# Kernel optimization log

Hardware: AMD Instinct MI355X
Metric: run time of the kernel (lower is better)

Reference implementation:

```python
import jax, jax.numpy as jnp
import numpy as np

NF = 64   # num_feat
DG = 8    # deformable_groups (also conv groups)
B, H, W = 4, 96, 96
K = 9     # 3x3 kernel positions


def _conv(x, w, b, padding=1, dilation=1, groups=1):
    out = jax.lax.conv_general_dilated(
        x, w, (1, 1), [(padding, padding), (padding, padding)],
        rhs_dilation=(dilation, dilation),
        dimension_numbers=('NCHW', 'OIHW', 'NCHW'),
        feature_group_count=groups)
    return out + b[None, :, None, None]


def _lrelu(t):
    return jnp.where(t >= 0, t, 0.1 * t)


def _cat_align(a, b):
    # channel-interleaved concat: [a0,b0,a1,b1,...]
    Bn, k, h, w = a.shape
    return jnp.stack([a, b], axis=2).reshape(Bn, 2 * k, h, w)


def _deform_conv(x, offset, mask, weight, bias, dilation, padding):
    # DCNv2 modulated deformable conv, stride 1.
    Bn, C, h, w = x.shape
    Cpg = C // DG
    off = offset.reshape(Bn, DG, K, 2, h, w)          # (dy, dx) per group/kernel pos
    m = mask.reshape(Bn, DG, K, h, w)
    ky = (jnp.repeat(jnp.arange(3), 3) * dilation - padding).astype(x.dtype)  # (K,)
    kx = (jnp.tile(jnp.arange(3), 3) * dilation - padding).astype(x.dtype)
    hs = jnp.arange(h, dtype=x.dtype)
    ws = jnp.arange(w, dtype=x.dtype)
    py = off[:, :, :, 0] + ky[None, None, :, None, None] + hs[None, None, None, :, None]
    px = off[:, :, :, 1] + kx[None, None, :, None, None] + ws[None, None, None, None, :]
    y0f = jnp.floor(py); x0f = jnp.floor(px)
    ly = (py - y0f)[:, :, None]  # broadcast over Cpg
    lx = (px - x0f)[:, :, None]
    y0 = y0f.astype(jnp.int32); x0 = x0f.astype(jnp.int32)
    xg = x.reshape(Bn, DG, Cpg, h * w)

    def gather(yi, xi):
        inb = ((yi >= 0) & (yi < h) & (xi >= 0) & (xi < w))
        idx = (jnp.clip(yi, 0, h - 1) * w + jnp.clip(xi, 0, w - 1)).reshape(Bn, DG, 1, K * h * w)
        v = jnp.take_along_axis(xg, jnp.broadcast_to(idx, (Bn, DG, Cpg, K * h * w)), axis=3)
        return v.reshape(Bn, DG, Cpg, K, h, w) * inb[:, :, None].astype(x.dtype)

    v00 = gather(y0, x0); v01 = gather(y0, x0 + 1)
    v10 = gather(y0 + 1, x0); v11 = gather(y0 + 1, x0 + 1)
    val = (v00 * (1 - ly) * (1 - lx) + v01 * (1 - ly) * lx
           + v10 * ly * (1 - lx) + v11 * ly * lx) * m[:, :, None]
    sampled = val.reshape(Bn, C, K, h, w)
    out = jnp.einsum('bckhw,ock->bohw', sampled, weight.reshape(weight.shape[0], C, K))
    return out + bias[None, :, None, None]


def _dcn(x, off_feat, om_w, om_b, w, b, dilation):
    pad = dilation  # int(3/2)*dilation
    out = _conv(off_feat, om_w, om_b, padding=pad, dilation=dilation)
    o1, o2, msk = jnp.split(out, 3, axis=1)
    offset = jnp.concatenate([o1, o2], axis=1)
    mask = jax.nn.sigmoid(msk)
    return _deform_conv(x, offset, mask, w, b, dilation, pad)


def setup_inputs() -> dict:
    key = jax.random.key(0)
    ks = iter(jax.random.split(key, 64))
    def rn(shape, s=0.05):
        return jax.random.normal(next(ks), shape, jnp.float32) * s
    d = {}
    d['nbr_feat'] = jax.random.normal(next(ks), (B, NF, H, W), jnp.float32)
    d['ref_feat'] = jax.random.normal(next(ks), (B, NF, H, W), jnp.float32)
    for lv, has3 in [('l3', False), ('l2', True), ('l1', True)]:
        d[f'oc1_w_{lv}'] = rn((NF, 2 * NF // DG, 3, 3)); d[f'oc1_b_{lv}'] = rn((NF,))
        oc2_in = 2 * NF if has3 else NF
        d[f'oc2_w_{lv}'] = rn((NF, oc2_in // DG, 3, 3)); d[f'oc2_b_{lv}'] = rn((NF,))
        if has3:
            d[f'oc3_w_{lv}'] = rn((NF, NF // DG, 3, 3)); d[f'oc3_b_{lv}'] = rn((NF,))
            d[f'fc_w_{lv}'] = rn((NF, 2 * NF // DG, 3, 3)); d[f'fc_b_{lv}'] = rn((NF,))
        d[f'om_w_{lv}'] = rn((DG * 3 * K, NF, 3, 3), 0.01); d[f'om_b_{lv}'] = rn((DG * 3 * K,), 0.01)
        d[f'dcn_w_{lv}'] = rn((NF, NF, 3, 3)); d[f'dcn_b_{lv}'] = rn((NF,))
    d['cas_oc1_w'] = rn((NF, 2 * NF // DG, 3, 3)); d['cas_oc1_b'] = rn((NF,))
    d['cas_oc2_w'] = rn((NF, NF // DG, 3, 3)); d['cas_oc2_b'] = rn((NF,))
    d['cas_om_w'] = rn((DG * 3 * K, NF, 3, 3), 0.01); d['cas_om_b'] = rn((DG * 3 * K,), 0.01)
    d['cas_w'] = rn((NF, NF, 3, 3)); d['cas_b'] = rn((NF,))
    return d


def reference(nbr_feat, ref_feat,
              oc1_w_l3, oc1_b_l3, oc2_w_l3, oc2_b_l3, om_w_l3, om_b_l3, dcn_w_l3, dcn_b_l3,
              oc1_w_l2, oc1_b_l2, oc2_w_l2, oc2_b_l2, oc3_w_l2, oc3_b_l2, fc_w_l2, fc_b_l2,
              om_w_l2, om_b_l2, dcn_w_l2, dcn_b_l2,
              oc1_w_l1, oc1_b_l1, oc2_w_l1, oc2_b_l1, oc3_w_l1, oc3_b_l1, fc_w_l1, fc_b_l1,
              om_w_l1, om_b_l1, dcn_w_l1, dcn_b_l1,
              cas_oc1_w, cas_oc1_b, cas_oc2_w, cas_oc2_b, cas_om_w, cas_om_b, cas_w, cas_b):
    # level 3 (dilation 5)
    off = _lrelu(_conv(_cat_align(nbr_feat, ref_feat), oc1_w_l3, oc1_b_l3, groups=DG))
    off = _lrelu(_conv(off, oc2_w_l3, oc2_b_l3, groups=DG))
    feat = _lrelu(_dcn(nbr_feat, off, om_w_l3, om_b_l3, dcn_w_l3, dcn_b_l3, 5))
    to, tf = off, feat
    # level 2 (dilation 3)
    off = _lrelu(_conv(_cat_align(nbr_feat, ref_feat), oc1_w_l2, oc1_b_l2, groups=DG))
    off = _lrelu(_conv(_cat_align(off, to), oc2_w_l2, oc2_b_l2, groups=DG))
    off = _lrelu(_conv(off, oc3_w_l2, oc3_b_l2, groups=DG))
    feat = _dcn(nbr_feat, off, om_w_l2, om_b_l2, dcn_w_l2, dcn_b_l2, 3)
    feat = _lrelu(_conv(_cat_align(feat, tf), fc_w_l2, fc_b_l2, groups=DG))
    to, tf = off, feat
    # level 1 (dilation 1), no lrelu on feat
    off = _lrelu(_conv(_cat_align(nbr_feat, ref_feat), oc1_w_l1, oc1_b_l1, groups=DG))
    off = _lrelu(_conv(_cat_align(off, to), oc2_w_l1, oc2_b_l1, groups=DG))
    off = _lrelu(_conv(off, oc3_w_l1, oc3_b_l1, groups=DG))
    feat = _dcn(nbr_feat, off, om_w_l1, om_b_l1, dcn_w_l1, dcn_b_l1, 1)
    feat = _conv(_cat_align(feat, tf), fc_w_l1, fc_b_l1, groups=DG)
    # cascade
    off = _cat_align(feat, ref_feat)
    off = _lrelu(_conv(_lrelu(_conv(off, cas_oc1_w, cas_oc1_b, groups=DG)), cas_oc2_w, cas_oc2_b, groups=DG))
    feat = _lrelu(_dcn(feat, off, cas_om_w, cas_om_b, cas_w, cas_b, 1))
    return feat
```

## Files before the change

kernel.cpp:

```cpp
#include <hip/hip_runtime.h>

#define BATCH 4
#define NFEAT 64
#define DGRP 8
#define HH 96
#define WW 96
#define HWP (HH*WW)

typedef short short4a __attribute__((ext_vector_type(4)));
typedef short short8 __attribute__((ext_vector_type(8)));
typedef float f32x4 __attribute__((ext_vector_type(4)));
typedef float f32x16 __attribute__((ext_vector_type(16)));

__device__ inline short f2bf(float f) {
  union { float f; unsigned u; } v; v.f = f;
  unsigned r = v.u + 0x7fff + ((v.u >> 16) & 1);
  return (short)(r >> 16);
}
__device__ inline float bf2f(short s) {
  return __uint_as_float(((unsigned)(unsigned short)s) << 16);
}

__global__ __launch_bounds__(256) void prep_om(
    const float* __restrict__ s0, const float* __restrict__ s1,
    const float* __restrict__ s2, const float* __restrict__ s3,
    short* __restrict__ dst) {
  int gid = blockIdx.x * 256 + threadIdx.x;
  if (gid >= 4 * 147456) return;
  int t = gid / 147456, r = gid % 147456;
  int tile = r / 18432, r2 = r % 18432;
  int kk = r2 / 512, r3 = r2 % 512;
  int lane = r3 / 8, j = r3 % 8;
  int col = lane & 31, half = lane >> 5;
  int oc = tile * 32 + col;
  int k = kk * 16 + half * 8 + j;
  int p = k >> 6, c = k & 63;
  const float* s = (t == 0) ? s0 : (t == 1) ? s1 : (t == 2) ? s2 : s3;
  float v = (oc < 216) ? s[(size_t)oc * 576 + c * 9 + p] : 0.f;
  dst[gid] = f2bf(v);
}

__global__ __launch_bounds__(256) void prep_dcnw(
    const float* __restrict__ s0, const float* __restrict__ s1,
    const float* __restrict__ s2, const float* __restrict__ s3,
    short* __restrict__ dst) {
  int gid = blockIdx.x * 256 + threadIdx.x;
  if (gid >= 4 * 36864) return;
  int t = gid / 36864, r = gid % 36864;
  int tile = r / 18432, r2 = r % 18432;
  int kk = r2 / 512, r3 = r2 % 512;
  int lane = r3 / 8, j = r3 % 8;
  int col = lane & 31, half = lane >> 5;
  int oc = tile * 32 + col;
  int k = kk * 16 + half * 8 + j;
  int p = k >> 6, c = k & 63;
  const float* s = (t == 0) ? s0 : (t == 1) ? s1 : (t == 2) ? s2 : s3;
  dst[gid] = f2bf(s[(size_t)oc * 576 + c * 9 + p]);
}

struct GwArgs {
  const float* src[12];
  int cat[12];
  int base[13];
};

__global__ __launch_bounds__(256) void prep_gw(GwArgs a, short* __restrict__ dst) {
  int gid = blockIdx.x * 256 + threadIdx.x;
  if (gid >= a.base[12]) return;
  int t = 0;
  while (gid >= a.base[t + 1]) ++t;
  int r = gid - a.base[t];
  const float* s = a.src[t];
  const int tsz = a.cat[t] ? 4608 : 2560;
  int tile = r / tsz, r2 = r % tsz;
  int kk = r2 / 512, r3 = r2 % 512;
  int lane = r3 >> 3, j = r3 & 7;
  int m = lane & 15, quad = lane >> 4;
  int oc = tile * 16 + m;
  int j32 = quad * 8 + j;
  float val = 0.f;
  if (a.cat[t]) {
    int gsel = j32 >> 4, ssel = (j32 >> 3) & 1, ch8 = j32 & 7;
    if (gsel == (m >> 3)) val = s[oc * 144 + (2 * ch8 + ssel) * 9 + kk];
  } else {
    int tapsel = j32 >> 4, gsel = (j32 >> 3) & 1, ch8 = j32 & 7;
    int p = 2 * kk + tapsel;
    if (p < 9 && gsel == (m >> 3)) val = s[oc * 72 + ch8 * 9 + p];
  }
  dst[gid] = f2bf(val);
}

__global__ __launch_bounds__(256) void transpose_bf16(
    const float* __restrict__ in, short* __restrict__ out) {
  __shared__ float s[64][65];
  const int p0 = blockIdx.x * 64;
  const int b = blockIdx.y;
  const int tx = threadIdx.x, ty = threadIdx.y;
  for (int c = ty; c < 64; c += 4)
    s[c][tx] = in[((size_t)b * NFEAT + c) * HWP + p0 + tx];
  __syncthreads();
  for (int p = ty; p < 64; p += 4)
    out[((size_t)b * HWP + p0 + p) * NFEAT + tx] = f2bf(s[tx][p]);
}

template <bool CAT, bool LRELU>
__global__ __launch_bounds__(256) void gconv_mfma(
    const short* __restrict__ in0, const short* __restrict__ in1,
    const short* __restrict__ Wsh, const float* __restrict__ bias,
    short* __restrict__ out) {
  const int lane = threadIdx.x, t = threadIdx.y;
  const int n = lane & 15, quad = lane >> 4;
  const int pixbase = blockIdx.x * 32;
  const int b = blockIdx.y;
  constexpr int NKK = CAT ? 9 : 5;

  short8 A[NKK];
#pragma unroll
  for (int kk = 0; kk < NKK; ++kk)
    A[kk] = *(const short8*)(Wsh + ((size_t)(t * NKK + kk) * 64 + lane) * 8);

  const short* sb;
  if (CAT) {
    sb = ((quad & 1) ? in1 : in0) + (size_t)b * HWP * 64 + (2 * t + (quad >> 1)) * 8;
  } else {
    sb = in0 + (size_t)b * HWP * 64 + (2 * t + (quad & 1)) * 8;
  }

  f32x4 acc[2] = {};
#pragma unroll
  for (int nt = 0; nt < 2; ++nt) {
    const int pix = pixbase + nt * 16 + n;
    const int yp = pix / WW, xp = pix % WW;
#pragma unroll
    for (int kk = 0; kk < NKK; ++kk) {
      const int p = CAT ? kk : (2 * kk + (quad >> 1));
      short8 B = {0, 0, 0, 0, 0, 0, 0, 0};
      if (p < 9) {
        const int sy = yp + p / 3 - 1, sx = xp + p % 3 - 1;
        if (((unsigned)sy < (unsigned)HH) && ((unsigned)sx < (unsigned)WW))
          B = *(const short8*)(sb + (size_t)(sy * WW + sx) * 64);
      }
      acc[nt] = __builtin_amdgcn_mfma_f32_16x16x32_bf16(A[kk], B, acc[nt], 0, 0, 0);
    }
  }

  const int ocb = t * 16 + quad * 4;
  const float b0 = bias[ocb], b1 = bias[ocb + 1], b2 = bias[ocb + 2], b3 = bias[ocb + 3];
#pragma unroll
  for (int nt = 0; nt < 2; ++nt) {
    float v0 = acc[nt][0] + b0, v1 = acc[nt][1] + b1;
    float v2 = acc[nt][2] + b2, v3 = acc[nt][3] + b3;
    if (LRELU) {
      v0 = (v0 >= 0.f) ? v0 : 0.1f * v0;
      v1 = (v1 >= 0.f) ? v1 : 0.1f * v1;
      v2 = (v2 >= 0.f) ? v2 : 0.1f * v2;
      v3 = (v3 >= 0.f) ? v3 : 0.1f * v3;
    }
    short4a pk = {f2bf(v0), f2bf(v1), f2bf(v2), f2bf(v3)};
    *(short4a*)(out + ((size_t)b * HWP + pixbase + nt * 16 + n) * 64 + ocb) = pk;
  }
}

#define BPITCH 324
template <int D>
__global__ __launch_bounds__(256) void omconv_mfma(
    const short* __restrict__ pixT,
    const short* __restrict__ Wsh,
    const float* __restrict__ bias,
    float* __restrict__ out) {
  const int lane = threadIdx.x;
  const int w = threadIdx.y;
  const int lid = w * 64 + lane;
  const int col = lane & 31, half = lane >> 5;
  const int pixbase = blockIdx.x * 64;
  const int b = blockIdx.y;

  __shared__ short Bs[64 * BPITCH];

  const short* aP0 = Wsh + ((size_t)(w * 36) * 64) * 8 + (size_t)lane * 8;
  const short* aP1 = Wsh + ((size_t)((w + 4) * 36) * 64) * 8 + (size_t)lane * 8;
  const short* pixb = pixT + (size_t)b * HWP * 64;

  f32x16 acc00 = {}, acc01 = {}, acc10 = {}, acc11 = {};

  for (int ph = 0; ph < 2; ++ph) {
    const int ntap = ph ? 4 : 5, pbase = ph ? 5 : 0, kbase = ph ? 20 : 0;
    if (ph) __syncthreads();
    const int nchunk = 64 * ntap * 8;
    for (int i = lid; i < nchunk; i += 256) {
      int row = i / (ntap * 8), q = i % (ntap * 8);
      int p = pbase + (q >> 3), c8 = q & 7;
      int pix = pixbase + row;
      int yp = pix / WW, xp = pix % WW;
      int sy = yp + (p / 3 - 1) * D, sx = xp + (p % 3 - 1) * D;
      short4a lo = {0, 0, 0, 0}, hi = {0, 0, 0, 0};
      if (((unsigned)sy < (unsigned)HH) && ((unsigned)sx < (unsigned)WW)) {
        const short* src = pixb + (size_t)(sy * WW + sx) * 64 + c8 * 8;
        lo = *(const short4a*)src;
        hi = *(const short4a*)(src + 4);
      }
      short* dst = Bs + row * BPITCH + q * 8;
      *(short4a*)dst = lo;
      *(short4a*)(dst + 4) = hi;
    }
    __syncthreads();

    const int nkk = ntap * 4;
#pragma unroll 4
    for (int kk = 0; kk < nkk; ++kk) {
      const int kkg = kbase + kk;
      short8 A0 = *(const short8*)(aP0 + (size_t)kkg * 512);
      short8 A1 = *(const short8*)(aP1 + (size_t)kkg * 512);
      const short* b0 = Bs + col * BPITCH + kk * 16 + half * 8;
      const short* b1 = Bs + (32 + col) * BPITCH + kk * 16 + half * 8;
      short4a l0 = *(const short4a*)b0, h0 = *(const short4a*)(b0 + 4);
      short4a l1 = *(const short4a*)b1, h1 = *(const short4a*)(b1 + 4);
      short8 B0 = {l0[0], l0[1], l0[2], l0[3], h0[0], h0[1], h0[2], h0[3]};
      short8 B1 = {l1[0], l1[1], l1[2], l1[3], h1[0], h1[1], h1[2], h1[3]};
      acc00 = __builtin_amdgcn_mfma_f32_32x32x16_bf16(A0, B0, acc00, 0, 0, 0);
      acc01 = __builtin_amdgcn_mfma_f32_32x32x16_bf16(A0, B1, acc01, 0, 0, 0);
      acc10 = __builtin_amdgcn_mfma_f32_32x32x16_bf16(A1, B0, acc10, 0, 0, 0);
      acc11 = __builtin_amdgcn_mfma_f32_32x32x16_bf16(A1, B1, acc11, 0, 0, 0);
    }
  }

  const int pix0 = pixbase + col, pix1 = pixbase + 32 + col;
#pragma unroll
  for (int r = 0; r < 16; ++r) {
    const int rrow = (r & 3) + 8 * (r >> 2) + 4 * half;
    const int oc0 = w * 32 + rrow;
    const int oc1 = (w + 4) * 32 + rrow;
    const float bs0 = bias[oc0];
    out[((size_t)b * 216 + oc0) * HWP + pix0] = acc00[r] + bs0;
    out[((size_t)b * 216 + oc0) * HWP + pix1] = acc01[r] + bs0;
    if (oc1 < 216) {
      const float bs1 = bias[oc1];
      out[((size_t)b * 216 + oc1) * HWP + pix0] = acc10[r] + bs1;
      out[((size_t)b * 216 + oc1) * HWP + pix1] = acc11[r] + bs1;
    }
  }
}

template <int D>
__global__ __launch_bounds__(256) void dcn_sample(
    const short* __restrict__ xT,
    const float* __restrict__ om,
    short* __restrict__ S) {
  const int px = threadIdx.x;
  const int dg = threadIdx.y;
  const int pb = blockIdx.x;
  const int b = blockIdx.y;
  const int pix = pb * 32 + px;
  const int yp = pix / WW, xp = pix % WW;
  const size_t bOM = (size_t)b * 216 * HWP;
  const short* xb = xT + (size_t)b * HWP * 64 + dg * 8;
  const int lane = (dg & 1) * 32 + px;
  short* Sp = S + (((size_t)(b * 288 + pb) * 36) * 64 + lane) * 8;

#pragma unroll
  for (int k = 0; k < 9; ++k) {
    float dy = om[bOM + (size_t)(dg * 18 + 2 * k) * HWP + pix];
    float dxv = om[bOM + (size_t)(dg * 18 + 2 * k + 1) * HWP + pix];
    float mr = om[bOM + (size_t)(144 + dg * 9 + k) * HWP + pix];
    float m = 1.f / (1.f + __expf(-mr));
    float py = (float)(yp + (k / 3 - 1) * D) + dy;
    float px_ = (float)(xp + (k % 3 - 1) * D) + dxv;
    float y0f = floorf(py), x0f = floorf(px_);
    float ly = py - y0f, lx = px_ - x0f;
    int y0 = (int)y0f, x0 = (int)x0f;
    int y1 = y0 + 1, x1 = x0 + 1;
    bool vy0 = (unsigned)y0 < (unsigned)HH, vy1 = (unsigned)y1 < (unsigned)HH;
    bool vx0 = (unsigned)x0 < (unsigned)WW, vx1 = (unsigned)x1 < (unsigned)WW;
    int cy0 = min(max(y0, 0), HH - 1), cy1 = min(max(y1, 0), HH - 1);
    int cx0 = min(max(x0, 0), WW - 1), cx1 = min(max(x1, 0), WW - 1);
    float w00 = (vy0 && vx0) ? (1.f - ly) * (1.f - lx) * m : 0.f;
    float w01 = (vy0 && vx1) ? (1.f - ly) * lx * m : 0.f;
    float w10 = (vy1 && vx0) ? ly * (1.f - lx) * m : 0.f;
    float w11 = (vy1 && vx1) ? ly * lx * m : 0.f;
    short8 s00 = *(const short8*)(xb + (size_t)(cy0 * WW + cx0) * 64);
    short8 s01 = *(const short8*)(xb + (size_t)(cy0 * WW + cx1) * 64);
    short8 s10 = *(const short8*)(xb + (size_t)(cy1 * WW + cx0) * 64);
    short8 s11 = *(const short8*)(xb + (size_t)(cy1 * WW + cx1) * 64);
    short8 pk;
#pragma unroll
    for (int cl = 0; cl < 8; ++cl) {
      float v = w00 * bf2f(s00[cl]) + w01 * bf2f(s01[cl]) +
                w10 * bf2f(s10[cl]) + w11 * bf2f(s11[cl]);
      pk[cl] = f2bf(v);
    }
    const int kk = k * 4 + (dg >> 1);
    *(short8*)(Sp + (size_t)kk * 512) = pk;
  }
}

template <bool LRELU, bool PMOUT>
__global__ __launch_bounds__(256) void dcn_gemm(
    const short* __restrict__ S,
    const short* __restrict__ Wd,
    const float* __restrict__ bias,
    void* __restrict__ outv) {
  const int lane = threadIdx.x;
  const int w = threadIdx.y;
  const int col = lane & 31, half = lane >> 5;
  const int octile = w & 1, kh = w >> 1;
  const int pb = blockIdx.x;
  const int b = blockIdx.y;
  const int pix = pb * 32 + col;

  const short* aP = Wd + ((size_t)(octile * 36) * 64 + lane) * 8;
  const short* bP = S + (((size_t)(b * 288 + pb) * 36) * 64 + lane) * 8;

  f32x16 acc = {};
#pragma unroll 6
  for (int kk = 0; kk < 18; ++kk) {
    const int kkg = kh * 18 + kk;
    short8 A = *(const short8*)(aP + (size_t)kkg * 512);
    short8 B = *(const short8*)(bP + (size_t)kkg * 512);
    acc = __builtin_amdgcn_mfma_f32_32x32x16_bf16(A, B, acc, 0, 0, 0);
  }

  __shared__ float red[2][64][17];
  if (kh == 1) {
#pragma unroll
    for (int r = 0; r < 16; ++r) red[octile][lane][r] = acc[r];
  }
  __syncthreads();
  if (kh == 0) {
    if (PMOUT) {
      short* out = (short*)outv;
#pragma unroll
      for (int rg = 0; rg < 4; ++rg) {
        short4a pk;
#pragma unroll
        for (int i = 0; i < 4; ++i) {
          const int r = rg * 4 + i;
          const int oc = octile * 32 + i + 8 * rg + 4 * half;
          float v = acc[r] + red[octile][lane][r] + bias[oc];
          if (LRELU) v = (v >= 0.f) ? v : 0.1f * v;
          pk[i] = f2bf(v);
        }
        *(short4a*)(out + ((size_t)b * HWP + pix) * 64 + octile * 32 + 8 * rg + 4 * half) = pk;
      }
    } else {
      float* out = (float*)outv;
#pragma unroll
      for (int r = 0; r < 16; ++r) {
        const int oc = octile * 32 + (r & 3) + 8 * (r >> 2) + 4 * half;
        float v = acc[r] + red[octile][lane][r] + bias[oc];
        if (LRELU) v = (v >= 0.f) ? v : 0.1f * v;
        out[((size_t)b * NFEAT + oc) * HWP + pix] = v;
      }
    }
  }
}

extern "C" void kernel_launch(void* const* d_in, const int* in_sizes, int n_in,
                              void* d_out, int out_size, void* d_ws, size_t ws_size,
                              hipStream_t stream) {
  const float* nbr = (const float*)d_in[0];
  const float* ref = (const float*)d_in[1];
  auto f = [&](int i) { return (const float*)d_in[i]; };

  float* ws = (float*)d_ws;
  const size_t PM = (size_t)BATCH * HWP * 64;
  float* omB = ws;
  short* sb = (short*)(ws + 7962624);
  short* refT = sb;
  short* pmA = refT + PM;
  short* pmB = pmA + PM;
  short* pmC = pmB + PM;
  short* pmD = pmC + PM;
  short* pmE = pmD + PM;
  short* Sbuf = pmE + PM;
  short* wbf = Sbuf + 21233664;
  short* wdcn = wbf + 589824;
  short* wgc = wdcn + 147456;
  short* nbrT = (short*)d_out;

  prep_om<<<(4 * 147456 + 255) / 256, 256, 0, stream>>>(f(6), f(18), f(30), f(38), wbf);
  prep_dcnw<<<(4 * 36864 + 255) / 256, 256, 0, stream>>>(f(8), f(20), f(32), f(40), wdcn);

  static const int gSrc[12] = {2, 4, 10, 12, 14, 16, 22, 24, 26, 28, 34, 36};
  static const int gCat[12] = {1, 0, 1, 1, 0, 1, 1, 1, 0, 1, 1, 0};
  GwArgs ga;
  int gb = 0;
  const short* wg[12];
  for (int t = 0; t < 12; ++t) {
    ga.src[t] = f(gSrc[t]);
    ga.cat[t] = gCat[t];
    ga.base[t] = gb;
    wg[t] = wgc + gb;
    gb += gCat[t] ? 18432 : 10240;
  }
  ga.base[12] = gb;
  prep_gw<<<(gb + 255) / 256, 256, 0, stream>>>(ga, wgc);

  short* wbf_l3 = wbf;
  short* wbf_l2 = wbf + 147456;
  short* wbf_l1 = wbf + 2 * 147456;
  short* wbf_cas = wbf + 3 * 147456;
  short* wd_l3 = wdcn;
  short* wd_l2 = wdcn + 36864;
  short* wd_l1 = wdcn + 2 * 36864;
  short* wd_cas = wdcn + 3 * 36864;

  dim3 gcGrid(288, BATCH), gcBlk(64, 4);
  dim3 omGrid(144, BATCH), omBlk(64, 4);
  dim3 smGrid(288, BATCH), smBlk(32, 8);
  dim3 dgGrid(288, BATCH), dgBlk(64, 4);
  dim3 trGrid(HWP / 64, BATCH), trBlk(64, 4);

  transpose_bf16<<<trGrid, trBlk, 0, stream>>>(nbr, nbrT);
  transpose_bf16<<<trGrid, trBlk, 0, stream>>>(ref, refT);

  gconv_mfma<true, true><<<gcGrid, gcBlk, 0, stream>>>(nbrT, refT, wg[0], f(3), pmA);
  gconv_mfma<false, true><<<gcGrid, gcBlk, 0, stream>>>(pmA, nullptr, wg[1], f(5), pmB);
  omconv_mfma<5><<<omGrid, omBlk, 0, stream>>>(pmB, wbf_l3, f(7), omB);
  dcn_sample<5><<<smGrid, smBlk, 0, stream>>>(nbrT, omB, Sbuf);
  dcn_gemm<true, true><<<dgGrid, dgBlk, 0, stream>>>(Sbuf, wd_l3, f(9), pmC);

  gconv_mfma<true, true><<<gcGrid, gcBlk, 0, stream>>>(nbrT, refT, wg[2], f(11), pmA);
  gconv_mfma<true, true><<<gcGrid, gcBlk, 0, stream>>>(pmA, pmB, wg[3], f(13), pmD);
  gconv_mfma<false, true><<<gcGrid, gcBlk, 0, stream>>>(pmD, nullptr, wg[4], f(15), pmE);
  omconv_mfma<3><<<omGrid, omBlk, 0, stream>>>(pmE, wbf_l2, f(19), omB);
  dcn_sample<3><<<smGrid, smBlk, 0, stream>>>(nbrT, omB, Sbuf);
  dcn_gemm<false, true><<<dgGrid, dgBlk, 0, stream>>>(Sbuf, wd_l2, f(21), pmD);
  gconv_mfma<true, true><<<gcGrid, gcBlk, 0, stream>>>(pmD, pmC, wg[5], f(17), pmA);

  gconv_mfma<true, true><<<gcGrid, gcBlk, 0, stream>>>(nbrT, refT, wg[6], f(23), pmC);
  gconv_mfma<true, true><<<gcGrid, gcBlk, 0, stream>>>(pmC, pmE, wg[7], f(25), pmD);
  gconv_mfma<false, true><<<gcGrid, gcBlk, 0, stream>>>(pmD, nullptr, wg[8], f(27), pmC);
  omconv_mfma<1><<<omGrid, omBlk, 0, stream>>>(pmC, wbf_l1, f(31), omB);
  dcn_sample<1><<<smGrid, smBlk, 0, stream>>>(nbrT, omB, Sbuf);
  dcn_gemm<false, true><<<dgGrid, dgBlk, 0, stream>>>(Sbuf, wd_l1, f(33), pmD);
  gconv_mfma<true, false><<<gcGrid, gcBlk, 0, stream>>>(pmD, pmA, wg[9], f(29), pmB);

  gconv_mfma<true, true><<<gcGrid, gcBlk, 0, stream>>>(pmB, refT, wg[10], f(35), pmC);
  gconv_mfma<false, true><<<gcGrid, gcBlk, 0, stream>>>(pmC, nullptr, wg[11], f(37), pmD);
  omconv_mfma<1><<<omGrid, omBlk, 0, stream>>>(pmD, wbf_cas, f(39), omB);
  dcn_sample<1><<<smGrid, smBlk, 0, stream>>>(pmB, omB, Sbuf);
  dcn_gemm<true, false><<<dgGrid, dgBlk, 0, stream>>>(Sbuf, wd_cas, f(41), (float*)d_out);
}
```

Baseline: 567.9 us.

## Fuse DCN sampling into GEMM via LDS and store offset/mask conv output as bf16

Merges the deformable sampling kernel and the DCN GEMM into one kernel that keeps the sampled columns for a 32-pixel tile in shared memory, so the large intermediate sample buffer no longer goes through global memory. The offset/mask conv now writes bf16 instead of fp32, which halves that traffic. The two input transposes are also merged into one launch using blockIdx.z. In exchange, the bf16 offsets and mask logits lose precision, which can shift the sampling positions slightly, and the added LDS may lower occupancy.

```diff
diff --git a/kernel.cpp b/kernel.cpp
--- a/kernel.cpp
+++ b/kernel.cpp
@@ -91,7 +91,10 @@
 }
 
 __global__ __launch_bounds__(256) void transpose_bf16(
-    const float* __restrict__ in, short* __restrict__ out) {
+    const float* __restrict__ in0, short* __restrict__ out0,
+    const float* __restrict__ in1, short* __restrict__ out1) {
+  const float* in = blockIdx.z ? in1 : in0;
+  short* out = blockIdx.z ? out1 : out0;
   __shared__ float s[64][65];
   const int p0 = blockIdx.x * 64;
   const int b = blockIdx.y;
@@ -167,7 +170,7 @@
     const short* __restrict__ pixT,
     const short* __restrict__ Wsh,
     const float* __restrict__ bias,
-    float* __restrict__ out) {
+    short* __restrict__ out) {
   const int lane = threadIdx.x;
   const int w = threadIdx.y;
   const int lid = w * 64 + lane;
@@ -231,84 +234,81 @@
     const int oc0 = w * 32 + rrow;
     const int oc1 = (w + 4) * 32 + rrow;
     const float bs0 = bias[oc0];
-    out[((size_t)b * 216 + oc0) * HWP + pix0] = acc00[r] + bs0;
-    out[((size_t)b * 216 + oc0) * HWP + pix1] = acc01[r] + bs0;
+    out[((size_t)b * 216 + oc0) * HWP + pix0] = f2bf(acc00[r] + bs0);
+    out[((size_t)b * 216 + oc0) * HWP + pix1] = f2bf(acc01[r] + bs0);
     if (oc1 < 216) {
       const float bs1 = bias[oc1];
-      out[((size_t)b * 216 + oc1) * HWP + pix0] = acc10[r] + bs1;
-      out[((size_t)b * 216 + oc1) * HWP + pix1] = acc11[r] + bs1;
-    }
-  }
-}
-
-template <int D>
-__global__ __launch_bounds__(256) void dcn_sample(
+      out[((size_t)b * 216 + oc1) * HWP + pix0] = f2bf(acc10[r] + bs1);
+      out[((size_t)b * 216 + oc1) * HWP + pix1] = f2bf(acc11[r] + bs1);
+    }
+  }
+}
+
+template <int D, bool LRELU, bool PMOUT>
+__global__ __launch_bounds__(256) void dcn_fused(
     const short* __restrict__ xT,
-    const float* __restrict__ om,
-    short* __restrict__ S) {
-  const int px = threadIdx.x;
-  const int dg = threadIdx.y;
-  const int pb = blockIdx.x;
-  const int b = blockIdx.y;
-  const int pix = pb * 32 + px;
-  const int yp = pix / WW, xp = pix % WW;
-  const size_t bOM = (size_t)b * 216 * HWP;
-  const short* xb = xT + (size_t)b * HWP * 64 + dg * 8;
-  const int lane = (dg & 1) * 32 + px;
-  short* Sp = S + (((size_t)(b * 288 + pb) * 36) * 64 + lane) * 8;
-
-#pragma unroll
-  for (int k = 0; k < 9; ++k) {
-    float dy = om[bOM + (size_t)(dg * 18 + 2 * k) * HWP + pix];
-    float dxv = om[bOM + (size_t)(dg * 18 + 2 * k + 1) * HWP + pix];
-    float mr = om[bOM + (size_t)(144 + dg * 9 + k) * HWP + pix];
-    float m = 1.f / (1.f + __expf(-mr));
-    float py = (float)(yp + (k / 3 - 1) * D) + dy;
-    float px_ = (float)(xp + (k % 3 - 1) * D) + dxv;
-    float y0f = floorf(py), x0f = floorf(px_);
-    float ly = py - y0f, lx = px_ - x0f;
-    int y0 = (int)y0f, x0 = (int)x0f;
-    int y1 = y0 + 1, x1 = x0 + 1;
-    bool vy0 = (unsigned)y0 < (unsigned)HH, vy1 = (unsigned)y1 < (unsigned)HH;
-    bool vx0 = (unsigned)x0 < (unsigned)WW, vx1 = (unsigned)x1 < (unsigned)WW;
-    int cy0 = min(max(y0, 0), HH - 1), cy1 = min(max(y1, 0), HH - 1);
-    int cx0 = min(max(x0, 0), WW - 1), cx1 = min(max(x1, 0), WW - 1);
-    float w00 = (vy0 && vx0) ? (1.f - ly) * (1.f - lx) * m : 0.f;
-    float w01 = (vy0 && vx1) ? (1.f - ly) * lx * m : 0.f;
-    float w10 = (vy1 && vx0) ? ly * (1.f - lx) * m : 0.f;
-    float w11 = (vy1 && vx1) ? ly * lx * m : 0.f;
-    short8 s00 = *(const short8*)(xb + (size_t)(cy0 * WW + cx0) * 64);
-    short8 s01 = *(const short8*)(xb + (size_t)(cy0 * WW + cx1) * 64);
-    short8 s10 = *(const short8*)(xb + (size_t)(cy1 * WW + cx0) * 64);
-    short8 s11 = *(const short8*)(xb + (size_t)(cy1 * WW + cx1) * 64);
-    short8 pk;
-#pragma unroll
-    for (int cl = 0; cl < 8; ++cl) {
-      float v = w00 * bf2f(s00[cl]) + w01 * bf2f(s01[cl]) +
-                w10 * bf2f(s10[cl]) + w11 * bf2f(s11[cl]);
-      pk[cl] = f2bf(v);
-    }
-    const int kk = k * 4 + (dg >> 1);
-    *(short8*)(Sp + (size_t)kk * 512) = pk;
-  }
-}
-
-template <bool LRELU, bool PMOUT>
-__global__ __launch_bounds__(256) void dcn_gemm(
-    const short* __restrict__ S,
+    const short* __restrict__ om,
     const short* __restrict__ Wd,
     const float* __restrict__ bias,
     void* __restrict__ outv) {
-  const int lane = threadIdx.x;
-  const int w = threadIdx.y;
+  __shared__ short Ls[36 * 512];
+  __shared__ float red[2][64][17];
+  const int tx = threadIdx.x, ty = threadIdx.y;
+  const int pb = blockIdx.x, b = blockIdx.y;
+
+  {
+    const int px = tx, dg = ty;
+    const int pix = pb * 32 + px;
+    const int yp = pix / WW, xp = pix % WW;
+    const size_t bOM = (size_t)b * 216 * HWP;
+    const short* xb = xT + (size_t)b * HWP * 64 + dg * 8;
+    short* Sp = Ls + (size_t)((dg & 1) * 32 + px) * 8;
+
+#pragma unroll
+    for (int k = 0; k < 9; ++k) {
+      float dy = bf2f(om[bOM + (size_t)(dg * 18 + 2 * k) * HWP + pix]);
+      float dxv = bf2f(om[bOM + (size_t)(dg * 18 + 2 * k + 1) * HWP + pix]);
+      float mr = bf2f(om[bOM + (size_t)(144 + dg * 9 + k) * HWP + pix]);
+      float m = 1.f / (1.f + __expf(-mr));
+      float py = (float)(yp + (k / 3 - 1) * D) + dy;
+      float px_ = (float)(xp + (k % 3 - 1) * D) + dxv;
+      float y0f = floorf(py), x0f = floorf(px_);
+      float ly = py - y0f, lx = px_ - x0f;
+      int y0 = (int)y0f, x0 = (int)x0f;
+      int y1 = y0 + 1, x1 = x0 + 1;
+      bool vy0 = (unsigned)y0 < (unsigned)HH, vy1 = (unsigned)y1 < (unsigned)HH;
+      bool vx0 = (unsigned)x0 < (unsigned)WW, vx1 = (unsigned)x1 < (unsigned)WW;
+      int cy0 = min(max(y0, 0), HH - 1), cy1 = min(max(y1, 0), HH - 1);
+      int cx0 = min(max(x0, 0), WW - 1), cx1 = min(max(x1, 0), WW - 1);
+      float w00 = (vy0 && vx0) ? (1.f - ly) * (1.f - lx) * m : 0.f;
+      float w01 = (vy0 && vx1) ? (1.f - ly) * lx * m : 0.f;
+      float w10 = (vy1 && vx0) ? ly * (1.f - lx) * m : 0.f;
+      float w11 = (vy1 && vx1) ? ly * lx * m : 0.f;
+      short8 s00 = *(const short8*)(xb + (size_t)(cy0 * WW + cx0) * 64);
+      short8 s01 = *(const short8*)(xb + (size_t)(cy0 * WW + cx1) * 64);
+      short8 s10 = *(const short8*)(xb + (size_t)(cy1 * WW + cx0) * 64);
+      short8 s11 = *(const short8*)(xb + (size_t)(cy1 * WW + cx1) * 64);
+      short8 pk;
+#pragma unroll
+      for (int cl = 0; cl < 8; ++cl) {
+        float v = w00 * bf2f(s00[cl]) + w01 * bf2f(s01[cl]) +
+                  w10 * bf2f(s10[cl]) + w11 * bf2f(s11[cl]);
+        pk[cl] = f2bf(v);
+      }
+      const int kk = k * 4 + (dg >> 1);
+      *(short8*)(Sp + (size_t)kk * 512) = pk;
+    }
+  }
+  __syncthreads();
+
+  const int lid = ty * 32 + tx;
+  const int lane = lid & 63, w = lid >> 6;
   const int col = lane & 31, half = lane >> 5;
   const int octile = w & 1, kh = w >> 1;
-  const int pb = blockIdx.x;
-  const int b = blockIdx.y;
   const int pix = pb * 32 + col;
 
   const short* aP = Wd + ((size_t)(octile * 36) * 64 + lane) * 8;
-  const short* bP = S + (((size_t)(b * 288 + pb) * 36) * 64 + lane) * 8;
+  const short* bP = Ls + (size_t)lane * 8;
 
   f32x16 acc = {};
 #pragma unroll 6
@@ -319,7 +319,6 @@
     acc = __builtin_amdgcn_mfma_f32_32x32x16_bf16(A, B, acc, 0, 0, 0);
   }
 
-  __shared__ float red[2][64][17];
   if (kh == 1) {
 #pragma unroll
     for (int r = 0; r < 16; ++r) red[octile][lane][r] = acc[r];
@@ -361,18 +360,16 @@
   const float* ref = (const float*)d_in[1];
   auto f = [&](int i) { return (const float*)d_in[i]; };
 
-  float* ws = (float*)d_ws;
+  short* s0 = (short*)d_ws;
   const size_t PM = (size_t)BATCH * HWP * 64;
-  float* omB = ws;
-  short* sb = (short*)(ws + 7962624);
-  short* refT = sb;
+  short* omB = s0;
+  short* refT = omB + 7962624;
   short* pmA = refT + PM;
   short* pmB = pmA + PM;
   short* pmC = pmB + PM;
   short* pmD = pmC + PM;
   short* pmE = pmD + PM;
-  short* Sbuf = pmE + PM;
-  short* wbf = Sbuf + 21233664;
+  short* wbf = pmE + PM;
   short* wdcn = wbf + 589824;
   short* wgc = wdcn + 147456;
   short* nbrT = (short*)d_out;
@@ -406,38 +403,32 @@
 
   dim3 gcGrid(288, BATCH), gcBlk(64, 4);
   dim3 omGrid(144, BATCH), omBlk(64, 4);
-  dim3 smGrid(288, BATCH), smBlk(32, 8);
-  dim3 dgGrid(288, BATCH), dgBlk(64, 4);
-  dim3 trGrid(HWP / 64, BATCH), trBlk(64, 4);
-
-  transpose_bf16<<<trGrid, trBlk, 0, stream>>>(nbr, nbrT);
-  transpose_bf16<<<trGrid, trBlk, 0, stream>>>(ref, refT);
+  dim3 dfGrid(288, BATCH), dfBlk(32, 8);
+  dim3 trGrid(HWP / 64, BATCH, 2), trBlk(64, 4);
+
+  transpose_bf16<<<trGrid, trBlk, 0, stream>>>(nbr, nbrT, ref, refT);
 
   gconv_mfma<true, true><<<gcGrid, gcBlk, 0, stream>>>(nbrT, refT, wg[0], f(3), pmA);
   gconv_mfma<false, true><<<gcGrid, gcBlk, 0, stream>>>(pmA, nullptr, wg[1], f(5), pmB);
   omconv_mfma<5><<<omGrid, omBlk, 0, stream>>>(pmB, wbf_l3, f(7), omB);
-  dcn_sample<5><<<smGrid, smBlk, 0, stream>>>(nbrT, omB, Sbuf);
-  dcn_gemm<true, true><<<dgGrid, dgBlk, 0, stream>>>(Sbuf, wd_l3, f(9), pmC);
+  dcn_fused<5, true, true><<<dfGrid, dfBlk, 0, stream>>>(nbrT, omB, wd_l3, f(9), pmC);
 
   gconv_mfma<true, true><<<gcGrid, gcBlk, 0, stream>>>(nbrT, refT, wg[2], f(11), pmA);
   gconv_mfma<true, true><<<gcGrid, gcBlk, 0, stream>>>(pmA, pmB, wg[3], f(13), pmD);
   gconv_mfma<false, true><<<gcGrid, gcBlk, 0, stream>>>(pmD, nullptr, wg[4], f(15), pmE);
   omconv_mfma<3><<<omGrid, omBlk, 0, stream>>>(pmE, wbf_l2, f(19), omB);
-  dcn_sample<3><<<smGrid, smBlk, 0, stream>>>(nbrT, omB, Sbuf);
-  dcn_gemm<false, true><<<dgGrid, dgBlk, 0, stream>>>(Sbuf, wd_l2, f(21), pmD);
+  dcn_fused<3, false, true><<<dfGrid, dfBlk, 0, stream>>>(nbrT, omB, wd_l2, f(21), pmD);
   gconv_mfma<true, true><<<gcGrid, gcBlk, 0, stream>>>(pmD, pmC, wg[5], f(17), pmA);
 
   gconv_mfma<true, true><<<gcGrid, gcBlk, 0, stream>>>(nbrT, refT, wg[6], f(23), pmC);
   gconv_mfma<true, true><<<gcGrid, gcBlk, 0, stream>>>(pmC, pmE, wg[7], f(25), pmD);
   gconv_mfma<false, true><<<gcGrid, gcBlk, 0, stream>>>(pmD, nullptr, wg[8], f(27), pmC);
   omconv_mfma<1><<<omGrid, omBlk, 0, stream>>>(pmC, wbf_l1, f(31), omB);
-  dcn_sample<1><<<smGrid, smBlk, 0, stream>>>(nbrT, omB, Sbuf);
-  dcn_gemm<false, true><<<dgGrid, dgBlk, 0, stream>>>(Sbuf, wd_l1, f(33), pmD);
+  dcn_fused<1, false, true><<<dfGrid, dfBlk, 0, stream>>>(nbrT, omB, wd_l1, f(33), pmD);
   gconv_mfma<true, false><<<gcGrid, gcBlk, 0, stream>>>(pmD, pmA, wg[9], f(29), pmB);
 
   gconv_mfma<true, true><<<gcGrid, gcBlk, 0, stream>>>(pmB, refT, wg[10], f(35), pmC);
   gconv_mfma<false, true><<<gcGrid, gcBlk, 0, stream>>>(pmC, nullptr, wg[11], f(37), pmD);
   omconv_mfma<1><<<omGrid, omBlk, 0, stream>>>(pmD, wbf_cas, f(39), omB);
-  dcn_sample<1><<<smGrid, smBlk, 0, stream>>>(pmB, omB, Sbuf);
-  dcn_gemm<true, false><<<dgGrid, dgBlk, 0, stream>>>(Sbuf, wd_cas, f(41), (float*)d_out);
-}
+  dcn_fused<1, true, false><<<dfGrid, dfBlk, 0, stream>>>(pmB, omB, wd_cas, f(41), (float*)d_out);
+}
```

After: 528.1 us. -7.0%, faster.
